# Kernel tuning notes

Hardware: AMD Instinct MI355X
Metric: run time of the kernel (lower is better)

## Reference

```python
import jax, jax.numpy as jnp
import numpy as np


def setup_inputs() -> dict:
    key = jax.random.key(0)
    k1, k2, k3 = jax.random.split(key, 3)
    B, D_IN, HIDDEN = 4096, 1024, 32768  # hidden = d_in * scale_size(32)
    x = jax.random.normal(k1, (B, D_IN), dtype=jnp.float32)
    W_enc = jax.random.normal(k2, (HIDDEN, D_IN), dtype=jnp.float32) * (1.0 / np.sqrt(D_IN))
    b_enc = jnp.zeros((HIDDEN,), dtype=jnp.float32)  # encoder.bias.data.zero_()
    # W_dec = encoder.weight.clone() then unit-norm rows (set_decoder_norm_to_unit_norm)
    W_dec = jax.random.normal(k3, (HIDDEN, D_IN), dtype=jnp.float32)
    W_dec = W_dec / (jnp.linalg.norm(W_dec, axis=1, keepdims=True) + jnp.finfo(jnp.float32).eps)
    b_dec = jnp.zeros((D_IN,), dtype=jnp.float32)
    return {"x": x, "W_enc": W_enc, "b_enc": b_enc, "W_dec": W_dec, "b_dec": b_dec, "k": 32}


def reference(x, W_enc, b_enc, W_dec, b_dec, k):
    # sae_in = x - b_dec; pre_acts = relu(encoder(sae_in))
    sae_in = x - b_dec
    pre_acts = jax.nn.relu(jnp.einsum('bd,hd->bh', sae_in, W_enc) + b_enc)  # [B, H]
    # topk_activation: keep top-k per row, zero elsewhere, then z @ W_dec.
    # Equivalent sparse decode: gather the k rows of W_dec and contract.
    topk_vals, topk_idx = jax.lax.top_k(pre_acts, k)  # [B, k]
    # x_reconstructed = z @ W_dec + b_dec  (z is the dense scatter of topk)
    x_rec = jnp.einsum('bk,bkd->bd', topk_vals, W_dec[topk_idx]) + b_dec
    return x_rec
```

## Files before the change

kernel.cpp:

```cpp
#include <hip/hip_runtime.h>
#include <hip/hip_bf16.h>
#include <stdint.h>
#include <stddef.h>


#define BROWS 4096
#define DIN   1024
#define HID   32768
#define KTOP  32
#define KC    48
#define PT    16

typedef short short8_t __attribute__((ext_vector_type(8)));
typedef float fx4 __attribute__((ext_vector_type(4)));

__device__ __forceinline__ unsigned short f2bf(float f) {
  unsigned u = __float_as_uint(f);
  u += 0x7FFFu + ((u >> 16) & 1u);
  return (unsigned short)(u >> 16);
}

__global__ __launch_bounds__(256) void conv_wc(const float* __restrict__ W,
                                               unsigned short* __restrict__ Wbc, int c0) {
  int base = (blockIdx.x * 256 + threadIdx.x) * 4;
  float4 v = *(const float4*)(W + (size_t)c0 * DIN + base);
  ushort4 o;
  o.x = f2bf(v.x); o.y = f2bf(v.y); o.z = f2bf(v.z); o.w = f2bf(v.w);
  *(ushort4*)(Wbc + base) = o;
}

__global__ __launch_bounds__(256) void prep_x(const float* __restrict__ x,
                                              const float* __restrict__ bdec,
                                              unsigned short* __restrict__ xbf) {
  int base = (blockIdx.x * 256 + threadIdx.x) * 4;
  int col = base & (DIN - 1);
  float4 xv = *(const float4*)(x + base);
  float4 bv = *(const float4*)(bdec + col);
  ushort4 o;
  o.x = f2bf(xv.x - bv.x); o.y = f2bf(xv.y - bv.y);
  o.z = f2bf(xv.z - bv.z); o.w = f2bf(xv.w - bv.w);
  *(ushort4*)(xbf + base) = o;
}

__global__ __launch_bounds__(256) void init_cand(unsigned* __restrict__ cand) {
  int i = blockIdx.x * 256 + threadIdx.x;
  if (i < BROWS * KC) cand[i] = 0u;
}

#define BM 128
#define BN 128
#define BK 64

__global__ __launch_bounds__(256) void gemm_scores(
    const unsigned short* __restrict__ A,
    const unsigned short* __restrict__ W,
    const float* __restrict__ benc,
    unsigned short* __restrict__ scores,
    int Hc, int c0) {
  __shared__ unsigned short As[BM * BK];
  __shared__ unsigned short Bs[BN * BK];

  const int t    = threadIdx.x;
  const int lane = t & 63;
  const int wv   = t >> 6;
  const int wm   = wv & 1;
  const int wn   = wv >> 1;
  const int l16  = lane & 15;
  const int quad = lane >> 4;

  const int row0  = blockIdx.y * BM;
  const int colc0 = blockIdx.x * BN;

  fx4 zero = {0.f, 0.f, 0.f, 0.f};
  fx4 acc[4][4];
#pragma unroll
  for (int i = 0; i < 4; ++i)
#pragma unroll
    for (int j = 0; j < 4; ++j) acc[i][j] = zero;

  const unsigned short* Abase = A + (size_t)row0 * DIN;
  const unsigned short* Wbase = W + (size_t)colc0 * DIN;

  int srow[4], spos[4], sk8[4];
#pragma unroll
  for (int r = 0; r < 4; ++r) {
    int c = r * 256 + t;
    srow[r] = c >> 3;
    sk8[r]  = c & 7;
    spos[r] = (c & 7) ^ (srow[r] & 7);
  }

  for (int k0 = 0; k0 < DIN; k0 += BK) {
    short8_t av[4], wvv[4];
#pragma unroll
    for (int r = 0; r < 4; ++r) {
      int gofs = srow[r] * DIN + k0 + sk8[r] * 8;
      av[r]  = *(const short8_t*)(Abase + gofs);
      wvv[r] = *(const short8_t*)(Wbase + gofs);
    }
#pragma unroll
    for (int r = 0; r < 4; ++r) {
      int lofs = srow[r] * BK + spos[r] * 8;
      *(short8_t*)(As + lofs) = av[r];
      *(short8_t*)(Bs + lofs) = wvv[r];
    }
    __syncthreads();
#pragma unroll
    for (int s = 0; s < BK / 32; ++s) {
      short8_t af[4], bfr[4];
      int pos = (((s * 4) + quad) ^ (l16 & 7)) * 8;
#pragma unroll
      for (int mt = 0; mt < 4; ++mt)
        af[mt] = *(const short8_t*)(As + (wm * 64 + mt * 16 + l16) * BK + pos);
#pragma unroll
      for (int nt = 0; nt < 4; ++nt)
        bfr[nt] = *(const short8_t*)(Bs + (wn * 64 + nt * 16 + l16) * BK + pos);
#pragma unroll
      for (int mt = 0; mt < 4; ++mt)
#pragma unroll
        for (int nt = 0; nt < 4; ++nt)
          acc[mt][nt] = __builtin_amdgcn_mfma_f32_16x16x32_bf16(af[mt], bfr[nt], acc[mt][nt], 0, 0, 0);
    }
    __syncthreads();
  }

#pragma unroll
  for (int nt = 0; nt < 4; ++nt) {
    int colc = colc0 + wn * 64 + nt * 16 + l16;
    float bv = benc[c0 + colc];
#pragma unroll
    for (int mt = 0; mt < 4; ++mt) {
      int rbase = row0 + wm * 64 + mt * 16 + quad * 4;
#pragma unroll
      for (int rg = 0; rg < 4; ++rg) {
        float v = acc[mt][nt][rg] + bv;
        scores[(size_t)(rbase + rg) * Hc + colc] = f2bf(v > 0.f ? v : 0.f);
      }
    }
  }
}

__global__ __launch_bounds__(128) void topk_cand(const unsigned short* __restrict__ scores,
                                                 int Hc, int c0,
                                                 unsigned* __restrict__ cand) {
  __shared__ unsigned lk[128 * 17];
  const int row = blockIdx.x;
  const int t = threadIdx.x;
  unsigned s[PT];
#pragma unroll
  for (int j = 0; j < PT; ++j) s[j] = 0u;

  const unsigned short* srow = scores + (size_t)row * Hc;
  for (int cb = t * 8; cb < Hc; cb += 128 * 8) {
    short8_t v = *(const short8_t*)(srow + cb);
    int gcb = c0 + cb;
#pragma unroll
    for (int e = 0; e < 8; ++e) {
      unsigned val = (unsigned)(unsigned short)v[e];
      unsigned key = (val << 16) | (unsigned)(0x7FFF - (gcb + e));
      if (key > s[PT - 1]) {
        unsigned prev = 0xFFFFFFFFu;
#pragma unroll
        for (int j = 0; j < PT; ++j) {
          unsigned sj = s[j];
          s[j] = (sj >= key) ? sj : (prev < key ? prev : key);
          prev = sj;
        }
      }
    }
  }
  if (t < KC) {
    unsigned key = cand[row * KC + t];
    if (key > s[PT - 1]) {
      unsigned prev = 0xFFFFFFFFu;
#pragma unroll
      for (int j = 0; j < PT; ++j) {
        unsigned sj = s[j];
        s[j] = (sj >= key) ? sj : (prev < key ? prev : key);
        prev = sj;
      }
    }
  }
#pragma unroll
  for (int j = 0; j < PT; ++j) lk[t * 17 + j] = s[j];
  __syncthreads();

  if (t < 64) {
    unsigned k0 = lk[t * 17];
    unsigned k1 = lk[(t + 64) * 17];
    int h0 = 0, h1 = 0;
    unsigned mywin = 0;
    for (int it = 0; it < KC; ++it) {
      unsigned wmax = (k0 > k1) ? k0 : k1;
#pragma unroll
      for (int off = 32; off >= 1; off >>= 1) {
        unsigned o = __shfl_down(wmax, (unsigned)off);
        if (o > wmax) wmax = o;
      }
      wmax = __shfl(wmax, 0);
      if (it == t) mywin = wmax;
      if (k0 == wmax)      { ++h0; k0 = (h0 < PT) ? lk[t * 17 + h0] : 0u; }
      else if (k1 == wmax) { ++h1; k1 = (h1 < PT) ? lk[(t + 64) * 17 + h1] : 0u; }
    }
    if (t < KC) cand[row * KC + t] = mywin;
  }
}

__global__ __launch_bounds__(256) void rescore_decode(
    const unsigned* __restrict__ cand,
    const float* __restrict__ x, const float* __restrict__ Wenc,
    const float* __restrict__ benc,
    const float* __restrict__ Wdec, const float* __restrict__ bdec,
    float* __restrict__ out) {
  __shared__ float xr[DIN];
  __shared__ double sc[KC];
  __shared__ int   scol[KC];
  __shared__ float fv[KTOP];
  __shared__ int   fi[KTOP];
  const int row = blockIdx.x, t = threadIdx.x;

  {
    float4 xv = *(const float4*)(x + (size_t)row * DIN + t * 4);
    float4 bv = *(const float4*)(bdec + t * 4);
    *(float4*)(xr + t * 4) = make_float4(xv.x - bv.x, xv.y - bv.y, xv.z - bv.z, xv.w - bv.w);
  }
  if (t < KC) scol[t] = 0x7FFF - (int)(cand[row * KC + t] & 0xFFFFu);
  if (t < KTOP) { fv[t] = 0.f; fi[t] = 0; }
  __syncthreads();

  const int wave = t >> 6, lane = t & 63;
  for (int j = wave; j < KC; j += 4) {
    int col = scol[j];
    const float* wr = Wenc + (size_t)col * DIN;
    double p = 0.0;
#pragma unroll
    for (int q = 0; q < 4; ++q) {
      int o = q * 256 + lane * 4;
      float4 w = *(const float4*)(wr + o);
      float4 xv = *(const float4*)(xr + o);
      p += (double)xv.x * (double)w.x + (double)xv.y * (double)w.y +
           (double)xv.z * (double)w.z + (double)xv.w * (double)w.w;
    }
#pragma unroll
    for (int off = 32; off >= 1; off >>= 1) p += __shfl_down(p, off);
    if (lane == 0) {
      double v = p + (double)benc[col];
      sc[j] = v > 0.0 ? v : 0.0;
    }
  }
  __syncthreads();

  if (t < KC) {
    double mv = sc[t];
    int mc = scol[t];
    int rank = 0;
    for (int j = 0; j < KC; ++j) {
      double oj = sc[j];
      if (oj > mv || (oj == mv && (scol[j] < mc || (scol[j] == mc && j < t)))) ++rank;
    }
    if (rank < KTOP) { fv[rank] = (float)mv; fi[rank] = mc; }
  }
  __syncthreads();

  const int c = t * 4;
  float4 bd = *(const float4*)(bdec + c);
  float a0 = bd.x, a1 = bd.y, a2 = bd.z, a3 = bd.w;
#pragma unroll 8
  for (int j = 0; j < KTOP; ++j) {
    float v = fv[j];
    float4 w = *(const float4*)(Wdec + (size_t)fi[j] * DIN + c);
    a0 += v * w.x; a1 += v * w.y; a2 += v * w.z; a3 += v * w.w;
  }
  *(float4*)(out + (size_t)row * DIN + c) = make_float4(a0, a1, a2, a3);
}

extern "C" void kernel_launch(void* const* d_in, const int* in_sizes, int n_in,
                              void* d_out, int out_size, void* d_ws, size_t ws_size,
                              hipStream_t stream) {
  const float* x    = (const float*)d_in[0];
  const float* Wenc = (const float*)d_in[1];
  const float* benc = (const float*)d_in[2];
  const float* Wdec = (const float*)d_in[3];
  const float* bdec = (const float*)d_in[4];
  float* out = (float*)d_out;

  char* ws = (char*)d_ws;
  unsigned short* xbf  = (unsigned short*)ws;
  unsigned*       cand = (unsigned*)(ws + (8u << 20));

  const size_t fixed = (size_t)(9u << 20);
  int Hc = HID;
  while (Hc > 128 &&
         fixed + (size_t)Hc * DIN * 2 + (size_t)BROWS * Hc * 2 > ws_size)
    Hc >>= 1;

  unsigned short* Wbc    = (unsigned short*)(ws + fixed);
  unsigned short* scores = (unsigned short*)(ws + fixed + (size_t)Hc * DIN * 2);

  prep_x<<<BROWS * DIN / 1024, 256, 0, stream>>>(x, bdec, xbf);
  init_cand<<<(BROWS * KC + 255) / 256, 256, 0, stream>>>(cand);
  for (int c0 = 0; c0 < HID; c0 += Hc) {
    conv_wc<<<Hc, 256, 0, stream>>>(Wenc, Wbc, c0);
    gemm_scores<<<dim3(Hc / BN, BROWS / BM), 256, 0, stream>>>(xbf, Wbc, benc, scores, Hc, c0);
    topk_cand<<<BROWS, 128, 0, stream>>>(scores, Hc, c0, cand);
  }
  rescore_decode<<<BROWS, 256, 0, stream>>>(cand, x, Wenc, benc, Wdec, bdec, out);
}
```

Baseline: 1.079 ms.

## Rewrite score GEMM with 256x256 tiles, direct-to-LDS double buffering and XCD swizzle

The bf16 score GEMM moves from 128x128 tiles with register-staged loads to 256x256 tiles with 8 waves. Each k-step is double-buffered in LDS and loaded with global_load_lds, interleaved with MFMA phases using barriers and s_setprio. Workgroups are remapped so neighbouring tiles share an XCD for L2 reuse, and the epilogue stages results through LDS to write coalesced 16-byte stores. It needs 128KB of dynamic LDS and more registers, so occupancy is limited and correctness depends on the hand-placed waitcnt and barriers.

New measurement: 1.119 ms. 1.04x slower.

```diff
diff --git a/kernel.cpp b/kernel.cpp
--- a/kernel.cpp
+++ b/kernel.cpp
@@ -10,6 +10,11 @@
 #define KTOP  32
 #define KC    48
 #define PT    16
+
+#define BM 256
+#define BN 256
+#define BK 64
+#define NT (DIN / BK)
 
 typedef short short8_t __attribute__((ext_vector_type(8)));
 typedef float fx4 __attribute__((ext_vector_type(4)));
@@ -47,94 +52,177 @@
   if (i < BROWS * KC) cand[i] = 0u;
 }
 
-#define BM 128
-#define BN 128
-#define BK 64
-
-__global__ __launch_bounds__(256) void gemm_scores(
+
+__device__ __forceinline__ void stage_half(const unsigned short* __restrict__ g0,
+                                           unsigned short* l0, int t, int k0) {
+  const int w6 = (t >> 6) << 6;
+#pragma unroll
+  for (int i = 0; i < 2; ++i) {
+    const int l  = i * 512 + t;
+    const int r  = l >> 3;
+    const int cl = (l & 7) ^ (r & 7);
+    const unsigned short* g = g0 + (size_t)r * DIN + k0 + cl * 8;
+    unsigned short* ld = l0 + (size_t)(i * 512 + w6) * 8;
+    __builtin_amdgcn_global_load_lds((const __attribute__((address_space(1))) unsigned int*)g,
+                                     (__attribute__((address_space(3))) unsigned int*)ld,
+                                     16, 0, 0);
+  }
+}
+
+__device__ __forceinline__ void tile_step(int tt,
+                                          const unsigned short* __restrict__ Ab,
+                                          const unsigned short* __restrict__ Wb,
+                                          unsigned short* bc, unsigned short* bn,
+                                          fx4 (&acc)[8][4],
+                                          int t, int l16, int quad, int wm, int wn) {
+  const int k1 = (tt + 1) * BK;
+  const int k2 = (tt + 2) * BK;
+  if (tt < NT - 1) { asm volatile("s_waitcnt vmcnt(4)" ::: "memory"); }
+  else             { asm volatile("s_waitcnt vmcnt(0)" ::: "memory"); }
+  __builtin_amdgcn_s_barrier();
+  const unsigned short* Ar = bc + wm * 8192;
+  const unsigned short* Br = bc + 16384;
+  short8_t a0[8], a1[8], bfv[4][2];
+#pragma unroll
+  for (int mt = 0; mt < 8; ++mt)
+    a0[mt] = *(const short8_t*)(Ar + (mt * 16 + l16) * 64 + ((quad) ^ (l16 & 7)) * 8);
+#pragma unroll
+  for (int nt = 0; nt < 4; ++nt)
+#pragma unroll
+    for (int ks = 0; ks < 2; ++ks)
+      bfv[nt][ks] = *(const short8_t*)(Br + (wn * 64 + nt * 16 + l16) * 64 +
+                                       ((ks * 4 + quad) ^ (l16 & 7)) * 8);
+  if (tt + 1 < NT) stage_half(Wb, bn + 16384, t, k1);
+  __builtin_amdgcn_s_setprio(1);
+#pragma unroll
+  for (int mt = 0; mt < 8; ++mt) {
+    acc[mt][0] = __builtin_amdgcn_mfma_f32_16x16x32_bf16(a0[mt], bfv[0][0], acc[mt][0], 0, 0, 0);
+    acc[mt][1] = __builtin_amdgcn_mfma_f32_16x16x32_bf16(a0[mt], bfv[1][0], acc[mt][1], 0, 0, 0);
+  }
+  __builtin_amdgcn_s_setprio(0);
+  __builtin_amdgcn_s_barrier();
+  if (tt + 1 < NT) stage_half(Wb + 128 * DIN, bn + 24576, t, k1);
+  __builtin_amdgcn_s_setprio(1);
+#pragma unroll
+  for (int mt = 0; mt < 8; ++mt) {
+    acc[mt][2] = __builtin_amdgcn_mfma_f32_16x16x32_bf16(a0[mt], bfv[2][0], acc[mt][2], 0, 0, 0);
+    acc[mt][3] = __builtin_amdgcn_mfma_f32_16x16x32_bf16(a0[mt], bfv[3][0], acc[mt][3], 0, 0, 0);
+  }
+  __builtin_amdgcn_s_setprio(0);
+  __builtin_amdgcn_s_barrier();
+#pragma unroll
+  for (int mt = 0; mt < 8; ++mt)
+    a1[mt] = *(const short8_t*)(Ar + (mt * 16 + l16) * 64 + ((4 + quad) ^ (l16 & 7)) * 8);
+#pragma unroll
+  for (int mt = 0; mt < 8; ++mt) { asm volatile("" : "+v"(a1[mt])); }
+  __builtin_amdgcn_sched_barrier(0);
+  __builtin_amdgcn_s_barrier();
+  if (tt + 2 < NT) stage_half(Ab, bc, t, k2);
+  __builtin_amdgcn_s_setprio(1);
+#pragma unroll
+  for (int mt = 0; mt < 8; ++mt) {
+    acc[mt][0] = __builtin_amdgcn_mfma_f32_16x16x32_bf16(a1[mt], bfv[0][1], acc[mt][0], 0, 0, 0);
+    acc[mt][1] = __builtin_amdgcn_mfma_f32_16x16x32_bf16(a1[mt], bfv[1][1], acc[mt][1], 0, 0, 0);
+  }
+  __builtin_amdgcn_s_setprio(0);
+  __builtin_amdgcn_s_barrier();
+  if (tt + 2 < NT) stage_half(Ab + 128 * DIN, bc + 8192, t, k2);
+  __builtin_amdgcn_s_setprio(1);
+#pragma unroll
+  for (int mt = 0; mt < 8; ++mt) {
+    acc[mt][2] = __builtin_amdgcn_mfma_f32_16x16x32_bf16(a1[mt], bfv[2][1], acc[mt][2], 0, 0, 0);
+    acc[mt][3] = __builtin_amdgcn_mfma_f32_16x16x32_bf16(a1[mt], bfv[3][1], acc[mt][3], 0, 0, 0);
+  }
+  __builtin_amdgcn_s_setprio(0);
+  __builtin_amdgcn_s_barrier();
+}
+
+__global__ __launch_bounds__(512, 2) void gemm_scores(
     const unsigned short* __restrict__ A,
     const unsigned short* __restrict__ W,
     const float* __restrict__ benc,
     unsigned short* __restrict__ scores,
     int Hc, int c0) {
-  __shared__ unsigned short As[BM * BK];
-  __shared__ unsigned short Bs[BN * BK];
-
+  extern __shared__ unsigned short lds[];
   const int t    = threadIdx.x;
   const int lane = t & 63;
   const int wv   = t >> 6;
-  const int wm   = wv & 1;
-  const int wn   = wv >> 1;
+  const int wm   = wv >> 2;
+  const int wn   = wv & 3;
   const int l16  = lane & 15;
   const int quad = lane >> 4;
 
-  const int row0  = blockIdx.y * BM;
-  const int colc0 = blockIdx.x * BN;
-
+  const int nwg  = (int)(gridDim.x * gridDim.y);
+  const int orig = (int)(blockIdx.y * gridDim.x + blockIdx.x);
+  const int q    = nwg >> 3, r8 = nwg & 7;
+  const int xcd  = orig & 7, loc = orig >> 3;
+  const int swz  = (xcd < r8 ? xcd * (q + 1) : r8 * (q + 1) + (xcd - r8) * q) + loc;
+  const int bx   = swz % (int)gridDim.x;
+  const int by   = swz / (int)gridDim.x;
+
+  const int row0  = by * BM;
+  const int colc0 = bx * BN;
+  const unsigned short* Ab = A + (size_t)row0 * DIN;
+  const unsigned short* Wb = W + (size_t)colc0 * DIN;
+
+  unsigned short* buf0 = lds;
+  unsigned short* buf1 = lds + 32768;
+
+  fx4 acc[8][4];
   fx4 zero = {0.f, 0.f, 0.f, 0.f};
-  fx4 acc[4][4];
-#pragma unroll
-  for (int i = 0; i < 4; ++i)
+#pragma unroll
+  for (int i = 0; i < 8; ++i)
 #pragma unroll
     for (int j = 0; j < 4; ++j) acc[i][j] = zero;
 
-  const unsigned short* Abase = A + (size_t)row0 * DIN;
-  const unsigned short* Wbase = W + (size_t)colc0 * DIN;
-
-  int srow[4], spos[4], sk8[4];
-#pragma unroll
-  for (int r = 0; r < 4; ++r) {
-    int c = r * 256 + t;
-    srow[r] = c >> 3;
-    sk8[r]  = c & 7;
-    spos[r] = (c & 7) ^ (srow[r] & 7);
-  }
-
-  for (int k0 = 0; k0 < DIN; k0 += BK) {
-    short8_t av[4], wvv[4];
-#pragma unroll
-    for (int r = 0; r < 4; ++r) {
-      int gofs = srow[r] * DIN + k0 + sk8[r] * 8;
-      av[r]  = *(const short8_t*)(Abase + gofs);
-      wvv[r] = *(const short8_t*)(Wbase + gofs);
-    }
-#pragma unroll
-    for (int r = 0; r < 4; ++r) {
-      int lofs = srow[r] * BK + spos[r] * 8;
-      *(short8_t*)(As + lofs) = av[r];
-      *(short8_t*)(Bs + lofs) = wvv[r];
-    }
+  stage_half(Ab,            buf0,         t, 0);
+  stage_half(Ab + 128*DIN,  buf0 + 8192,  t, 0);
+  stage_half(Wb,            buf0 + 16384, t, 0);
+  stage_half(Wb + 128*DIN,  buf0 + 24576, t, 0);
+  stage_half(Ab,            buf1,         t, BK);
+  stage_half(Ab + 128*DIN,  buf1 + 8192,  t, BK);
+
+#pragma unroll 1
+  for (int it = 0; it < NT / 2; ++it) {
+    tile_step(2 * it,     Ab, Wb, buf0, buf1, acc, t, l16, quad, wm, wn);
+    tile_step(2 * it + 1, Ab, Wb, buf1, buf0, acc, t, l16, quad, wm, wn);
+  }
+
+  const int colbase = colc0 + wn * 64;
+  float bval[4];
+#pragma unroll
+  for (int nt = 0; nt < 4; ++nt) bval[nt] = benc[c0 + colbase + nt * 16 + l16];
+
+  unsigned short* et = lds;
+#pragma unroll
+  for (int c = 0; c < 2; ++c) {
     __syncthreads();
-#pragma unroll
-    for (int s = 0; s < BK / 32; ++s) {
-      short8_t af[4], bfr[4];
-      int pos = (((s * 4) + quad) ^ (l16 & 7)) * 8;
-#pragma unroll
-      for (int mt = 0; mt < 4; ++mt)
-        af[mt] = *(const short8_t*)(As + (wm * 64 + mt * 16 + l16) * BK + pos);
-#pragma unroll
-      for (int nt = 0; nt < 4; ++nt)
-        bfr[nt] = *(const short8_t*)(Bs + (wn * 64 + nt * 16 + l16) * BK + pos);
-#pragma unroll
-      for (int mt = 0; mt < 4; ++mt)
-#pragma unroll
-        for (int nt = 0; nt < 4; ++nt)
-          acc[mt][nt] = __builtin_amdgcn_mfma_f32_16x16x32_bf16(af[mt], bfr[nt], acc[mt][nt], 0, 0, 0);
+    if (wm == c) {
+#pragma unroll
+      for (int mt = 0; mt < 8; ++mt)
+#pragma unroll
+        for (int nt = 0; nt < 4; ++nt) {
+          const int col = wn * 64 + nt * 16 + l16;
+          const int ch = col >> 3, cw = col & 7;
+#pragma unroll
+          for (int rg = 0; rg < 4; ++rg) {
+            const int row = mt * 16 + quad * 4 + rg;
+            float v = acc[mt][nt][rg] + bval[nt];
+            et[row * 256 + ((ch ^ quad) * 8) + cw] = f2bf(v > 0.f ? v : 0.f);
+          }
+        }
     }
     __syncthreads();
-  }
-
-#pragma unroll
-  for (int nt = 0; nt < 4; ++nt) {
-    int colc = colc0 + wn * 64 + nt * 16 + l16;
-    float bv = benc[c0 + colc];
-#pragma unroll
-    for (int mt = 0; mt < 4; ++mt) {
-      int rbase = row0 + wm * 64 + mt * 16 + quad * 4;
-#pragma unroll
-      for (int rg = 0; rg < 4; ++rg) {
-        float v = acc[mt][nt][rg] + bv;
-        scores[(size_t)(rbase + rg) * Hc + colc] = f2bf(v > 0.f ? v : 0.f);
+    {
+      const int row = t >> 2;
+      const int cb  = (t & 3) * 8;
+      const int xq  = (row >> 2) & 3;
+      const size_t gro = (size_t)(row0 + c * 128 + row) * Hc + colc0;
+#pragma unroll
+      for (int i = 0; i < 8; ++i) {
+        const int ch = cb + i;
+        short8_t v = *(const short8_t*)(et + row * 256 + ((ch ^ xq) * 8));
+        *(short8_t*)(scores + gro + ch * 8) = v;
       }
     }
   }
@@ -290,18 +378,25 @@
 
   const size_t fixed = (size_t)(9u << 20);
   int Hc = HID;
-  while (Hc > 128 &&
+  while (Hc > 256 &&
          fixed + (size_t)Hc * DIN * 2 + (size_t)BROWS * Hc * 2 > ws_size)
     Hc >>= 1;
 
   unsigned short* Wbc    = (unsigned short*)(ws + fixed);
   unsigned short* scores = (unsigned short*)(ws + fixed + (size_t)Hc * DIN * 2);
+
+  static bool attr_set = false;
+  if (!attr_set) {
+    (void)hipFuncSetAttribute((const void*)gemm_scores,
+                              hipFuncAttributeMaxDynamicSharedMemorySize, 131072);
+    attr_set = true;
+  }
 
   prep_x<<<BROWS * DIN / 1024, 256, 0, stream>>>(x, bdec, xbf);
   init_cand<<<(BROWS * KC + 255) / 256, 256, 0, stream>>>(cand);
   for (int c0 = 0; c0 < HID; c0 += Hc) {
     conv_wc<<<Hc, 256, 0, stream>>>(Wenc, Wbc, c0);
-    gemm_scores<<<dim3(Hc / BN, BROWS / BM), 256, 0, stream>>>(xbf, Wbc, benc, scores, Hc, c0);
+    gemm_scores<<<dim3(Hc / BN, BROWS / BM), 512, 131072, stream>>>(xbf, Wbc, benc, scores, Hc, c0);
     topk_cand<<<BROWS, 128, 0, stream>>>(scores, Hc, c0, cand);
   }
   rescore_decode<<<BROWS, 256, 0, stream>>>(cand, x, Wenc, benc, Wdec, bdec, out);
```
